# Kernel optimization log

Hardware: AMD Instinct MI355X
Metric: run time of the kernel (lower is better)

The kernel has to match this reference:

```python
import jax, jax.numpy as jnp
import numpy as np

B, G = 32, 8          # batch, num_genres
N, T = 64, 64         # notes_size, timestep_size (input)
D, O = 32, 32         # notes_out, timestep_out (output)


def setup_inputs() -> dict:
    key = jax.random.key(0)
    k1, k2, k3, k4, k5 = jax.random.split(key, 5)
    x = jax.random.normal(k1, (B, N, T), dtype=jnp.float32)
    y = jax.random.uniform(k2, (B, G), dtype=jnp.float32)
    weight = jax.random.normal(k3, (G, D, O, N, T), dtype=jnp.float32) * 0.02
    bias = jax.random.normal(k4, (D * O,), dtype=jnp.float32) * 0.02
    mask = jax.random.randint(k5, (O, T), 0, 2).astype(jnp.float32)
    return {"x": x, "y": y, "weight": weight, "bias": bias, "mask": mask}


def reference(x, y, weight, bias, mask):
    # Fused form of:
    #   mw  = einsum('gdont,ot->gdont', weight, mask)
    #   mw2 = einsum('gdont,bg->bdont', mw, y)      # huge intermediate avoided
    #   out = einsum('bnt,bdont->bdo', x, mw2) + bias
    mw = weight * mask[None, None, :, None, :]          # (g,d,o,n,t)
    xw = jnp.einsum('bnt,gdont->bgdo', x, mw)           # contract n,t first
    out = jnp.einsum('bg,bgdo->bdo', y, xw)             # (b,d,o)
    return out + bias.reshape(D, O)[None, :, :]
```

## Files before the change

kernel.cpp:

```cpp
#include <hip/hip_runtime.h>
#include <hip/hip_bf16.h>

typedef __bf16 bf16x8 __attribute__((ext_vector_type(8)));
typedef float f32x4 __attribute__((ext_vector_type(4)));

#define G 8
#define B 32
#define D 32
#define O 32
#define K 4096
#define T 64
#define KSPLIT 2
#define KCHUNK (K / KSPLIT)
#define BK 256
#define NSTEP (KCHUNK / BK)

#define XB_ELEMS (B * K)
#define S_ELEMS  (KSPLIT * G * D * O * B)

__global__ __launch_bounds__(256) void prep_xb(const float* __restrict__ x,
                                               __bf16* __restrict__ xb) {
    int tid = blockIdx.x * 256 + threadIdx.x;
    int kt = tid >> 7;
    int b  = (tid >> 2) & 31;
    int c  = tid & 3;
    int k  = kt * 32 + c * 8;
    const float4 x0 = *(const float4*)(x + b * K + k);
    const float4 x1 = *(const float4*)(x + b * K + k + 4);
    bf16x8 r;
    r[0] = (__bf16)x0.x; r[1] = (__bf16)x0.y; r[2] = (__bf16)x0.z; r[3] = (__bf16)x0.w;
    r[4] = (__bf16)x1.x; r[5] = (__bf16)x1.y; r[6] = (__bf16)x1.z; r[7] = (__bf16)x1.w;
    *(bf16x8*)(xb + (size_t)tid * 8) = r;
}

__global__ __launch_bounds__(256) void gemm_main(const float* __restrict__ W,
                                                 const __bf16* __restrict__ xb,
                                                 const float* __restrict__ mask,
                                                 float* __restrict__ S) {
    __shared__ float ldsW[2][32 * BK];
    const int d  = blockIdx.x, g = blockIdx.y, ks = blockIdx.z;
    const int wid  = threadIdx.x >> 6;
    const int lane = threadIdx.x & 63;
    const int bh = wid & 1, oh = wid >> 1;
    const int l15 = lane & 15, g16 = lane >> 4;

    const int r = oh * 16 + l15;
    const int lds_ro = r * 1024 + ((g16 * 32) ^ ((r & 7) * 16));

    const float* mrow = mask + r * T + g16 * 8;
    const float4 me0 = *(const float4*)(mrow);
    const float4 me1 = *(const float4*)(mrow + 4);
    const float4 mo0 = *(const float4*)(mrow + 32);
    const float4 mo1 = *(const float4*)(mrow + 36);

    const __bf16* xbl = xb + (size_t)(ks * (KCHUNK / 32)) * 1024
                           + (bh * 16 + l15) * 32 + g16 * 8;

    const size_t wrow0 = ((size_t)(g * D + d) * O + 8 * wid) * K + (size_t)ks * KCHUNK;

    f32x4 acc = {0.f, 0.f, 0.f, 0.f};

#define STAGE(buf, step)                                                          \
    {                                                                             \
        _Pragma("unroll")                                                         \
        for (int i = 0; i < 8; ++i) {                                             \
            const int row = 8 * wid + i;                                          \
            const char* src = (const char*)(W + wrow0 + (size_t)i * K             \
                                            + (size_t)(step) * BK)                \
                              + ((lane * 16) ^ (i * 16));                         \
            __builtin_amdgcn_global_load_lds(                                     \
                (const __attribute__((address_space(1))) void*)src,               \
                (__attribute__((address_space(3))) void*)((char*)&ldsW[buf][0]    \
                                                          + row * 1024),          \
                16, 0, 0);                                                        \
        }                                                                         \
    }

    STAGE(0, 0);
    __syncthreads();

    int cur = 0;
    for (int step = 0; step < NSTEP; ++step) {
        if (step + 1 < NSTEP) STAGE(cur ^ 1, step + 1);

        const char* lb = (const char*)&ldsW[cur][0];
        const __bf16* xs = xbl + (size_t)(step * 8) * 1024;
        #pragma unroll
        for (int s = 0; s < 8; ++s) {
            const int a0 = lds_ro + s * 128;
            const f32x4 alo = *(const f32x4*)(lb + a0);
            const f32x4 ahi = *(const f32x4*)(lb + (a0 ^ 16));
            const float4 ms0 = (s & 1) ? mo0 : me0;
            const float4 ms1 = (s & 1) ? mo1 : me1;
            bf16x8 af;
            af[0] = (__bf16)(alo[0] * ms0.x); af[1] = (__bf16)(alo[1] * ms0.y);
            af[2] = (__bf16)(alo[2] * ms0.z); af[3] = (__bf16)(alo[3] * ms0.w);
            af[4] = (__bf16)(ahi[0] * ms1.x); af[5] = (__bf16)(ahi[1] * ms1.y);
            af[6] = (__bf16)(ahi[2] * ms1.z); af[7] = (__bf16)(ahi[3] * ms1.w);
            const bf16x8 bfr = *(const bf16x8*)(xs + (size_t)s * 1024);
            acc = __builtin_amdgcn_mfma_f32_16x16x32_bf16(af, bfr, acc, 0, 0, 0);
        }
        __syncthreads();
        cur ^= 1;
    }
#undef STAGE

    float* Sp = S + (((size_t)(ks * G + g) * D + d) * O + oh * 16) * B + bh * 16;
    #pragma unroll
    for (int i = 0; i < 4; ++i)
        Sp[(g16 * 4 + i) * B + l15] = acc[i];
}

__global__ __launch_bounds__(256) void reduce_out(const float* __restrict__ S,
                                                  const float* __restrict__ y,
                                                  const float* __restrict__ bias,
                                                  float* __restrict__ out) {
    int tid = blockIdx.x * 256 + threadIdx.x;
    int d = tid >> 10, o = (tid >> 5) & 31, b = tid & 31;
    float acc = bias[d * O + o];
    #pragma unroll
    for (int g = 0; g < G; ++g) {
        float s = S[(size_t)g * (D * O * B) + tid]
                + S[(size_t)(G + g) * (D * O * B) + tid];
        acc += y[b * G + g] * s;
    }
    out[b * (D * O) + d * O + o] = acc;
}

extern "C" void kernel_launch(void* const* d_in, const int* in_sizes, int n_in,
                              void* d_out, int out_size, void* d_ws, size_t ws_size,
                              hipStream_t stream) {
    const float* x    = (const float*)d_in[0];
    const float* y    = (const float*)d_in[1];
    const float* w    = (const float*)d_in[2];
    const float* bias = (const float*)d_in[3];
    const float* mask = (const float*)d_in[4];
    float* out = (float*)d_out;

    __bf16* xbp = (__bf16*)d_ws;
    float*  S   = (float*)((char*)d_ws + (size_t)XB_ELEMS * sizeof(__bf16));

    prep_xb<<<64, 256, 0, stream>>>(x, xbp);
    gemm_main<<<dim3(D, G, KSPLIT), 256, 0, stream>>>(w, xbp, mask, S);
    reduce_out<<<128, 256, 0, stream>>>(S, y, bias, out);
}
```

Measured before the change: 36.54 us.

## Fuse reduction into GEMM epilogue via atomics and split blocks over o-halves

Drops the separate reduce kernel and the partial-sum scratch buffer. The GEMM epilogue now scales its accumulator by y and atomically adds into the output, which a combined prep kernel pre-initialises with the bias. GEMM blocks are halved to 128 threads with 16 weight rows each, doubling the grid to 1024 blocks for more parallelism and less LDS per block. The cost is 16-way atomic contention per output element (8 genres times 2 K-splits) and a summation order that is no longer deterministic.

Measured after the change: 35.16 us. -3.8%, faster.

```diff
diff --git a/kernel.cpp b/kernel.cpp
--- a/kernel.cpp
+++ b/kernel.cpp
@@ -14,40 +14,46 @@
 #define KCHUNK (K / KSPLIT)
 #define BK 256
 #define NSTEP (KCHUNK / BK)
+#define MROWS 16
 
 #define XB_ELEMS (B * K)
-#define S_ELEMS  (KSPLIT * G * D * O * B)
 
-__global__ __launch_bounds__(256) void prep_xb(const float* __restrict__ x,
-                                               __bf16* __restrict__ xb) {
+__global__ __launch_bounds__(256) void prep_and_init(const float* __restrict__ x,
+                                                     const float* __restrict__ bias,
+                                                     __bf16* __restrict__ xb,
+                                                     float* __restrict__ out) {
     int tid = blockIdx.x * 256 + threadIdx.x;
-    int kt = tid >> 7;
-    int b  = (tid >> 2) & 31;
-    int c  = tid & 3;
-    int k  = kt * 32 + c * 8;
-    const float4 x0 = *(const float4*)(x + b * K + k);
-    const float4 x1 = *(const float4*)(x + b * K + k + 4);
-    bf16x8 r;
-    r[0] = (__bf16)x0.x; r[1] = (__bf16)x0.y; r[2] = (__bf16)x0.z; r[3] = (__bf16)x0.w;
-    r[4] = (__bf16)x1.x; r[5] = (__bf16)x1.y; r[6] = (__bf16)x1.z; r[7] = (__bf16)x1.w;
-    *(bf16x8*)(xb + (size_t)tid * 8) = r;
+    if (tid < 16384) {
+        int b = (tid >> 2) & 31;
+        int k = (tid >> 7) * 32 + (tid & 3) * 8;
+        const float4 x0 = *(const float4*)(x + b * K + k);
+        const float4 x1 = *(const float4*)(x + b * K + k + 4);
+        bf16x8 r;
+        r[0] = (__bf16)x0.x; r[1] = (__bf16)x0.y; r[2] = (__bf16)x0.z; r[3] = (__bf16)x0.w;
+        r[4] = (__bf16)x1.x; r[5] = (__bf16)x1.y; r[6] = (__bf16)x1.z; r[7] = (__bf16)x1.w;
+        *(bf16x8*)(xb + (size_t)tid * 8) = r;
+    } else {
+        int t2 = tid - 16384;
+        out[t2] = bias[t2 & 1023];
+    }
 }
 
-__global__ __launch_bounds__(256) void gemm_main(const float* __restrict__ W,
+__global__ __launch_bounds__(128) void gemm_main(const float* __restrict__ W,
                                                  const __bf16* __restrict__ xb,
                                                  const float* __restrict__ mask,
-                                                 float* __restrict__ S) {
-    __shared__ float ldsW[2][32 * BK];
-    const int d  = blockIdx.x, g = blockIdx.y, ks = blockIdx.z;
+                                                 const float* __restrict__ y,
+                                                 float* __restrict__ out) {
+    __shared__ float ldsW[2][MROWS * BK];
+    const int d = blockIdx.x, g = blockIdx.y;
+    const int oh = blockIdx.z & 1, ks = blockIdx.z >> 1;
     const int wid  = threadIdx.x >> 6;
     const int lane = threadIdx.x & 63;
-    const int bh = wid & 1, oh = wid >> 1;
+    const int bh = wid;
     const int l15 = lane & 15, g16 = lane >> 4;
 
-    const int r = oh * 16 + l15;
-    const int lds_ro = r * 1024 + ((g16 * 32) ^ ((r & 7) * 16));
+    const int lds_ro = l15 * 1024 + ((g16 * 32) ^ ((l15 & 7) * 16));
 
-    const float* mrow = mask + r * T + g16 * 8;
+    const float* mrow = mask + (oh * 16 + l15) * T + g16 * 8;
     const float4 me0 = *(const float4*)(mrow);
     const float4 me1 = *(const float4*)(mrow + 4);
     const float4 mo0 = *(const float4*)(mrow + 32);
@@ -56,7 +62,8 @@
     const __bf16* xbl = xb + (size_t)(ks * (KCHUNK / 32)) * 1024
                            + (bh * 16 + l15) * 32 + g16 * 8;
 
-    const size_t wrow0 = ((size_t)(g * D + d) * O + 8 * wid) * K + (size_t)ks * KCHUNK;
+    const size_t wrow0 = ((size_t)(g * D + d) * O + oh * 16 + 8 * wid) * K
+                         + (size_t)ks * KCHUNK;
 
     f32x4 acc = {0.f, 0.f, 0.f, 0.f};
 
@@ -105,26 +112,12 @@
     }
 #undef STAGE
 
-    float* Sp = S + (((size_t)(ks * G + g) * D + d) * O + oh * 16) * B + bh * 16;
+    const int bg = bh * 16 + l15;
+    const float yv = y[bg * G + g];
+    float* op = out + bg * (D * O) + d * O + oh * 16;
     #pragma unroll
     for (int i = 0; i < 4; ++i)
-        Sp[(g16 * 4 + i) * B + l15] = acc[i];
-}
-
-__global__ __launch_bounds__(256) void reduce_out(const float* __restrict__ S,
-                                                  const float* __restrict__ y,
-                                                  const float* __restrict__ bias,
-                                                  float* __restrict__ out) {
-    int tid = blockIdx.x * 256 + threadIdx.x;
-    int d = tid >> 10, o = (tid >> 5) & 31, b = tid & 31;
-    float acc = bias[d * O + o];
-    #pragma unroll
-    for (int g = 0; g < G; ++g) {
-        float s = S[(size_t)g * (D * O * B) + tid]
-                + S[(size_t)(G + g) * (D * O * B) + tid];
-        acc += y[b * G + g] * s;
-    }
-    out[b * (D * O) + d * O + o] = acc;
+        unsafeAtomicAdd(op + g16 * 4 + i, yv * acc[i]);
 }
 
 extern "C" void kernel_launch(void* const* d_in, const int* in_sizes, int n_in,
@@ -138,9 +131,7 @@
     float* out = (float*)d_out;
 
     __bf16* xbp = (__bf16*)d_ws;
-    float*  S   = (float*)((char*)d_ws + (size_t)XB_ELEMS * sizeof(__bf16));
 
-    prep_xb<<<64, 256, 0, stream>>>(x, xbp);
-    gemm_main<<<dim3(D, G, KSPLIT), 256, 0, stream>>>(w, xbp, mask, S);
-    reduce_out<<<128, 256, 0, stream>>>(S, y, bias, out);
+    prep_and_init<<<192, 256, 0, stream>>>(x, bias, xbp, out);
+    gemm_main<<<dim3(D, G, 4), 128, 0, stream>>>(w, xbp, mask, y, out);
 }
```
